# Kernel optimization log

Measured on AMD Instinct MI355X. Metric: run time of the kernel, lower is better.

The kernel has to match this reference:

```python
import jax, jax.numpy as jnp
import numpy as np

N, E, H, XD, ED, YD, L = 10000, 640000, 128, 8, 8, 112, 4
EPS_MSG = 1e-7   # GENConv message eps
EPS_SM = 1e-16   # pyg softmax denom eps
EPS_LN = 1e-5    # layernorm eps


def node_ln(x, g, b):
    # torch.nn.LayerNorm over last dim
    m = x.mean(axis=-1, keepdims=True)
    v = x.var(axis=-1, keepdims=True)
    return (x - m) * jax.lax.rsqrt(v + EPS_LN) * g + b


def graph_ln(x, g, b):
    # pyg LayerNorm mode='graph' (no batch): global mean/std over all nodes+channels
    xc = x - x.mean()
    std = jnp.sqrt((xc * xc).mean())
    return xc / (std + EPS_LN) * g + b


def setup_inputs() -> dict:
    key = jax.random.key(0)
    ks = jax.random.split(key, 10)
    rn = lambda k, s, sc: jax.random.normal(k, s, jnp.float32) * sc
    return {
        "x": jax.random.normal(ks[0], (N, XD), jnp.float32),
        "edge_index": jax.random.randint(ks[1], (2, E), 0, N),
        "edge_attr": jax.random.normal(ks[2], (E, ED), jnp.float32),
        "Wn": rn(ks[3], (XD, H), 0.3), "bn": jnp.zeros((H,), jnp.float32),
        "We": rn(ks[4], (ED, H), 0.3), "be": jnp.zeros((H,), jnp.float32),
        "t": jnp.ones((L,), jnp.float32),
        "W1": rn(ks[5], (L, H, 2 * H), 0.08), "b1": jnp.zeros((L, 2 * H), jnp.float32),
        "g1": jnp.ones((L, 2 * H), jnp.float32), "bt1": jnp.zeros((L, 2 * H), jnp.float32),
        "W2": rn(ks[6], (L, 2 * H, H), 0.08), "b2": jnp.zeros((L, H), jnp.float32),
        "lng": jnp.ones((L, H), jnp.float32), "lnb": jnp.zeros((L, H), jnp.float32),
        "Wout": rn(ks[7], (H, YD), 0.08), "bout": jnp.zeros((YD,), jnp.float32),
    }


def reference(x, edge_index, edge_attr, Wn, bn, We, be, t, W1, b1, g1, bt1,
              W2, b2, lng, lnb, Wout, bout):
    src, dst = edge_index[0], edge_index[1]
    h = x @ Wn + bn                       # [N,H] node encoder
    ea = edge_attr @ We + be              # [E,H] edge encoder

    def gen_conv(h, i):
        msg = jax.nn.relu(h[src] + ea) + EPS_MSG          # [E,H]
        logit = msg * t[i]
        mx = jax.ops.segment_max(logit, dst, num_segments=N)
        ex = jnp.exp(logit - mx[dst])
        den = jax.ops.segment_sum(ex, dst, num_segments=N)
        alpha = ex / (den[dst] + EPS_SM)
        agg = jax.ops.segment_sum(alpha * msg, dst, num_segments=N) + h  # root add
        z = jax.nn.relu(graph_ln(agg @ W1[i] + b1[i], g1[i], bt1[i]))
        return z @ W2[i] + b2[i]

    h = gen_conv(h, 0)                    # first layer: conv only
    for i in range(1, L):                 # res+ blocks (dropout off: eval)
        r = jax.nn.relu(node_ln(h, lng[i], lnb[i]))
        h = h + gen_conv(r, i)
    h = jax.nn.relu(node_ln(h, lng[0], lnb[0]))  # layers[0].act(layers[0].norm(x))
    return h @ Wout + bout
```

## Files before the change

kernel.cpp:

```cpp
#include <hip/hip_runtime.h>
#include <math.h>

#define NN 10000
#define NE 640000
#define H 128
#define H2 256
#define XD 8
#define ED 8
#define YD 112
#define NL 4
#define EPS_MSG 1e-7f
#define EPS_SM 1e-16f
#define EPS_LN 1e-5f
#define TM 8
#define NB1 (NN / TM)
#define TNO 16
#define NBO (NN / TNO)

typedef _Float16 h2 __attribute__((ext_vector_type(2)));

__global__ void hist_k(const int* __restrict__ dst, int* __restrict__ counts) {
    int e = blockIdx.x * 256 + threadIdx.x;
    if (e < NE) atomicAdd(&counts[dst[e]], 1);
}

__global__ void scan_k(const int* __restrict__ counts, int* __restrict__ rowptr) {
    __shared__ int part[1024];
    int tid = threadIdx.x;
    const int CH = (NN + 1023) / 1024;
    int base = tid * CH;
    int s = 0;
    for (int j = 0; j < CH; j++) { int i = base + j; if (i < NN) s += counts[i]; }
    part[tid] = s; __syncthreads();
    for (int off = 1; off < 1024; off <<= 1) {
        int v = (tid >= off) ? part[tid - off] : 0;
        __syncthreads();
        part[tid] += v;
        __syncthreads();
    }
    int run = part[tid] - s;
    for (int j = 0; j < CH; j++) {
        int i = base + j;
        if (i < NN) { rowptr[i] = run; run += counts[i]; }
    }
    if (tid == 1023) rowptr[NN] = run;
}

__global__ void scatter_k(const int* __restrict__ dst, const int* __restrict__ rowptr,
                          int* __restrict__ fill, int* __restrict__ perm) {
    int e = blockIdx.x * 256 + threadIdx.x;
    if (e >= NE) return;
    int d = dst[e];
    int pos = rowptr[d] + atomicAdd(&fill[d], 1);
    perm[pos] = e;
}

__global__ void pack_k(const int* __restrict__ perm, const int* __restrict__ src,
                       const float* __restrict__ eattr, int* __restrict__ srcs,
                       _Float16* __restrict__ eacsr) {
    int pos = blockIdx.x * 256 + threadIdx.x;
    if (pos >= NE) return;
    int e = perm[pos];
    srcs[pos] = src[e];
    const float4* ein = (const float4*)eattr;
    float4 a = ein[(size_t)e * 2];
    float4 b = ein[(size_t)e * 2 + 1];
    float4 pack;
    _Float16* pp = (_Float16*)&pack;
    pp[0] = (_Float16)a.x; pp[1] = (_Float16)a.y; pp[2] = (_Float16)a.z; pp[3] = (_Float16)a.w;
    pp[4] = (_Float16)b.x; pp[5] = (_Float16)b.y; pp[6] = (_Float16)b.z; pp[7] = (_Float16)b.w;
    ((float4*)eacsr)[pos] = pack;
}

__global__ void node_enc_k(const float* __restrict__ x, const float* __restrict__ Wn,
                           const float* __restrict__ bn, float* __restrict__ h) {
    int n = blockIdx.x, c = threadIdx.x;
    __shared__ float xl[XD];
    if (c < XD) xl[c] = x[n * XD + c];
    __syncthreads();
    float acc = bn[c];
#pragma unroll
    for (int k = 0; k < XD; k++) acc = fmaf(xl[k], Wn[k * H + c], acc);
    h[(size_t)n * H + c] = acc;
}

__global__ void __launch_bounds__(64) edge_agg_k(
    const float* __restrict__ rin, const int* __restrict__ rowptr,
    const int* __restrict__ srcs, const _Float16* __restrict__ eacsr,
    const float* __restrict__ We, const float* __restrict__ be,
    const float* __restrict__ tptr, int layer, float* __restrict__ agg) {
    int n = blockIdx.x, c = threadIdx.x;
    h2 wA[4], wB[4];
#pragma unroll
    for (int k = 0; k < 4; k++) {
        wA[k][0] = (_Float16)We[(2 * k) * H + c];
        wA[k][1] = (_Float16)We[(2 * k + 1) * H + c];
        wB[k][0] = (_Float16)We[(2 * k) * H + c + 64];
        wB[k][1] = (_Float16)We[(2 * k + 1) * H + c + 64];
    }
    float becA = be[c], becB = be[c + 64];
    float ts2 = tptr[layer] * 1.44269504088896f;
    int beg = rowptr[n], end = rowptr[n + 1];
    const float* rn0 = rin + (size_t)n * H + c;
    float rvA = rn0[0], rvB = rn0[64];
    float denA = 0.f, numA = 0.f, denB = 0.f, numB = 0.f;
#pragma unroll 4
    for (int j = beg; j < end; ++j) {
        int sn = srcs[j];
        float4 raw = *(const float4*)(eacsr + (size_t)j * ED);
        const h2* ep = (const h2*)&raw;
        const float* hp = rin + (size_t)sn * H + c;
        float hvA = hp[0], hvB = hp[64];
        float pA = __builtin_amdgcn_fdot2(ep[0], wA[0], becA, false);
        pA = __builtin_amdgcn_fdot2(ep[1], wA[1], pA, false);
        pA = __builtin_amdgcn_fdot2(ep[2], wA[2], pA, false);
        pA = __builtin_amdgcn_fdot2(ep[3], wA[3], pA, false);
        float pB = __builtin_amdgcn_fdot2(ep[0], wB[0], becB, false);
        pB = __builtin_amdgcn_fdot2(ep[1], wB[1], pB, false);
        pB = __builtin_amdgcn_fdot2(ep[2], wB[2], pB, false);
        pB = __builtin_amdgcn_fdot2(ep[3], wB[3], pB, false);
        float msgA = fmaxf(hvA + pA, 0.f) + EPS_MSG;
        float msgB = fmaxf(hvB + pB, 0.f) + EPS_MSG;
        float peA = __builtin_amdgcn_exp2f(msgA * ts2);
        float peB = __builtin_amdgcn_exp2f(msgB * ts2);
        denA += peA; numA = fmaf(peA, msgA, numA);
        denB += peB; numB = fmaf(peB, msgB, numB);
    }
    float* ao = agg + (size_t)n * H + c;
    ao[0]  = numA / (denA + EPS_SM) + rvA;
    ao[64] = numB / (denB + EPS_SM) + rvB;
}

__global__ void __launch_bounds__(256) mm1_k(const float* __restrict__ agg,
    const float* __restrict__ W1i, const float* __restrict__ b1i,
    float* __restrict__ y1, float* __restrict__ part) {
    int nb = blockIdx.x, o = threadIdx.x;
    int n0 = nb * TM;
    __shared__ float a[TM][H];
    {
        const float4* ag4 = (const float4*)(agg + (size_t)n0 * H);
        float4* a4 = (float4*)a;
        a4[o] = ag4[o];
    }
    __syncthreads();
    float acc[TM];
#pragma unroll
    for (int i = 0; i < TM; i++) acc[i] = 0.f;
    for (int k = 0; k < H; k += 4) {
        float w0 = W1i[k * H2 + o];
        float w1 = W1i[(k + 1) * H2 + o];
        float w2 = W1i[(k + 2) * H2 + o];
        float w3 = W1i[(k + 3) * H2 + o];
#pragma unroll
        for (int i = 0; i < TM; i++) {
            float4 av = *(const float4*)&a[i][k];
            acc[i] = fmaf(av.x, w0, acc[i]);
            acc[i] = fmaf(av.y, w1, acc[i]);
            acc[i] = fmaf(av.z, w2, acc[i]);
            acc[i] = fmaf(av.w, w3, acc[i]);
        }
    }
    float bo = b1i[o];
    float ps = 0.f, ps2 = 0.f;
#pragma unroll
    for (int i = 0; i < TM; i++) {
        float v = acc[i] + bo;
        y1[(size_t)(n0 + i) * H2 + o] = v;
        ps += v; ps2 += v * v;
    }
#pragma unroll
    for (int off = 32; off; off >>= 1) { ps += __shfl_xor(ps, off); ps2 += __shfl_xor(ps2, off); }
    __shared__ float red[8];
    int w = o >> 6;
    if ((o & 63) == 0) { red[w] = ps; red[4 + w] = ps2; }
    __syncthreads();
    if (o == 0) {
        part[nb * 2]     = red[0] + red[1] + red[2] + red[3];
        part[nb * 2 + 1] = red[4] + red[5] + red[6] + red[7];
    }
}

__global__ void __launch_bounds__(256) mm2_k(const float* __restrict__ y1,
    const float* __restrict__ g1i, const float* __restrict__ bt1i,
    const float* __restrict__ W2i, const float* __restrict__ b2i,
    const float* __restrict__ part, float* __restrict__ h,
    const float* __restrict__ lgp, const float* __restrict__ lbp,
    float* __restrict__ r, int first) {
    int nb = blockIdx.x, tid = threadIdx.x;
    int o = tid & 127, half = tid >> 7;
    int rb = half * 4;
    int n0 = nb * TM;
    float s = 0.f, s2 = 0.f;
    for (int i = tid; i < NB1; i += 256) { s += part[2 * i]; s2 += part[2 * i + 1]; }
#pragma unroll
    for (int off = 32; off; off >>= 1) { s += __shfl_xor(s, off); s2 += __shfl_xor(s2, off); }
    __shared__ float sred[8];
    int w4 = tid >> 6;
    if ((tid & 63) == 0) { sred[w4] = s; sred[4 + w4] = s2; }
    __syncthreads();
    const float M = (float)NN * (float)H2;
    float m = (sred[0] + sred[1] + sred[2] + sred[3]) / M;
    float var = fmaxf((sred[4] + sred[5] + sred[6] + sred[7]) / M - m * m, 0.f);
    float istd = 1.f / (sqrtf(var) + EPS_LN);

    __shared__ float z[TM][H2];
    __syncthreads();
    {
        const float4* y4 = (const float4*)(y1 + (size_t)n0 * H2);
        const float4* g4 = (const float4*)g1i;
        const float4* b4 = (const float4*)bt1i;
        float4* z4 = (float4*)z;
#pragma unroll
        for (int t = tid; t < TM * H2 / 4; t += 256) {
            int k4 = t & 63;
            float4 v = y4[t];
            float4 g = g4[k4], b = b4[k4];
            v.x = fmaxf((v.x - m) * istd * g.x + b.x, 0.f);
            v.y = fmaxf((v.y - m) * istd * g.y + b.y, 0.f);
            v.z = fmaxf((v.z - m) * istd * g.z + b.z, 0.f);
            v.w = fmaxf((v.w - m) * istd * g.w + b.w, 0.f);
            z4[t] = v;
        }
    }
    __syncthreads();
    float acc[4];
#pragma unroll
    for (int i = 0; i < 4; i++) acc[i] = 0.f;
    for (int k = 0; k < H2; k += 4) {
        float w0 = W2i[k * H + o];
        float w1 = W2i[(k + 1) * H + o];
        float w2 = W2i[(k + 2) * H + o];
        float w3 = W2i[(k + 3) * H + o];
#pragma unroll
        for (int i = 0; i < 4; i++) {
            float4 zv = *(const float4*)&z[rb + i][k];
            acc[i] = fmaf(zv.x, w0, acc[i]);
            acc[i] = fmaf(zv.y, w1, acc[i]);
            acc[i] = fmaf(zv.z, w2, acc[i]);
            acc[i] = fmaf(zv.w, w3, acc[i]);
        }
    }
    float bo = b2i[o];
    float vv[4];
#pragma unroll
    for (int i = 0; i < 4; i++) {
        size_t idx = (size_t)(n0 + rb + i) * H + o;
        float v = acc[i] + bo;
        if (!first) v += h[idx];
        h[idx] = v;
        vv[i] = v;
    }
    __shared__ float rs[2][2][4], rs2[2][2][4];
    int w2i_ = (tid >> 6) & 1;
#pragma unroll
    for (int i = 0; i < 4; i++) {
        float ss = vv[i], ss2 = vv[i] * vv[i];
#pragma unroll
        for (int off = 32; off; off >>= 1) { ss += __shfl_xor(ss, off); ss2 += __shfl_xor(ss2, off); }
        if ((tid & 63) == 0) { rs[half][w2i_][i] = ss; rs2[half][w2i_][i] = ss2; }
    }
    __syncthreads();
    float gc = lgp[o], bc = lbp[o];
#pragma unroll
    for (int i = 0; i < 4; i++) {
        float S = rs[half][0][i] + rs[half][1][i];
        float S2 = rs2[half][0][i] + rs2[half][1][i];
        float mn = S * (1.f / H);
        float vr = S2 * (1.f / H) - mn * mn;
        float inv = rsqrtf(vr + EPS_LN);
        float ov = (vv[i] - mn) * inv * gc + bc;
        r[(size_t)(n0 + rb + i) * H + o] = fmaxf(ov, 0.f);
    }
}

__global__ void __launch_bounds__(128) mmout_k(const float* __restrict__ r,
    const float* __restrict__ Wout, const float* __restrict__ bout,
    float* __restrict__ out) {
    int nb = blockIdx.x, o = threadIdx.x;
    int n0 = nb * TNO;
    __shared__ float a[TNO][H];
    {
        const float4* r4 = (const float4*)(r + (size_t)n0 * H);
        float4* a4 = (float4*)a;
        for (int t = o; t < TNO * H / 4; t += 128) a4[t] = r4[t];
    }
    __syncthreads();
    if (o < YD) {
        float acc[TNO];
#pragma unroll
        for (int i = 0; i < TNO; i++) acc[i] = 0.f;
        for (int k = 0; k < H; k += 4) {
            float w0 = Wout[k * YD + o];
            float w1 = Wout[(k + 1) * YD + o];
            float w2 = Wout[(k + 2) * YD + o];
            float w3 = Wout[(k + 3) * YD + o];
#pragma unroll
            for (int i = 0; i < TNO; i++) {
                float4 av = *(const float4*)&a[i][k];
                acc[i] = fmaf(av.x, w0, acc[i]);
                acc[i] = fmaf(av.y, w1, acc[i]);
                acc[i] = fmaf(av.z, w2, acc[i]);
                acc[i] = fmaf(av.w, w3, acc[i]);
            }
        }
        float bo = bout[o];
#pragma unroll
        for (int i = 0; i < TNO; i++) out[(size_t)(n0 + i) * YD + o] = acc[i] + bo;
    }
}

extern "C" void kernel_launch(void* const* d_in, const int* in_sizes, int n_in,
                              void* d_out, int out_size, void* d_ws, size_t ws_size,
                              hipStream_t stream) {
    const float* x    = (const float*)d_in[0];
    const int*   ei   = (const int*)d_in[1];
    const float* eattr= (const float*)d_in[2];
    const float* Wn   = (const float*)d_in[3];
    const float* bn   = (const float*)d_in[4];
    const float* We   = (const float*)d_in[5];
    const float* be   = (const float*)d_in[6];
    const float* t    = (const float*)d_in[7];
    const float* W1   = (const float*)d_in[8];
    const float* b1   = (const float*)d_in[9];
    const float* g1   = (const float*)d_in[10];
    const float* bt1  = (const float*)d_in[11];
    const float* W2   = (const float*)d_in[12];
    const float* b2   = (const float*)d_in[13];
    const float* lng  = (const float*)d_in[14];
    const float* lnb  = (const float*)d_in[15];
    const float* Wout = (const float*)d_in[16];
    const float* bout = (const float*)d_in[17];
    float* out = (float*)d_out;

    const int* src = ei;
    const int* dst = ei + NE;

    char* ws = (char*)d_ws;
    size_t off = 0;
    auto alloc = [&](size_t bytes) -> char* {
        char* p = ws + off;
        off += (bytes + 255) & ~(size_t)255;
        return p;
    };
    int*      counts = (int*)alloc((size_t)NN * 2 * 4);
    int*      fill   = counts + NN;
    int*      rowptr = (int*)alloc((size_t)(NN + 1) * 4);
    int*      perm   = (int*)alloc((size_t)NE * 4);
    int*      srcs   = (int*)alloc((size_t)NE * 4);
    _Float16* eacsr  = (_Float16*)alloc((size_t)NE * ED * 2);
    float*    h      = (float*)alloc((size_t)NN * H * 4);
    float*    r      = (float*)alloc((size_t)NN * H * 4);
    float*    agg    = (float*)alloc((size_t)NN * H * 4);
    float*    y1     = (float*)alloc((size_t)NN * H2 * 4);
    float*    part   = (float*)alloc((size_t)NB1 * 2 * 4);
    (void)ws_size; (void)in_sizes; (void)n_in; (void)out_size;

    hipMemsetAsync(counts, 0, (size_t)NN * 2 * 4, stream);

    hist_k<<<(NE + 255) / 256, 256, 0, stream>>>(dst, counts);
    scan_k<<<1, 1024, 0, stream>>>(counts, rowptr);
    scatter_k<<<(NE + 255) / 256, 256, 0, stream>>>(dst, rowptr, fill, perm);
    pack_k<<<(NE + 255) / 256, 256, 0, stream>>>(perm, src, eattr, srcs, eacsr);
    node_enc_k<<<NN, H, 0, stream>>>(x, Wn, bn, h);

    for (int i = 0; i < NL; i++) {
        const float* cin = (i == 0) ? h : r;
        edge_agg_k<<<NN, 64, 0, stream>>>(cin, rowptr, srcs, eacsr, We, be, t, i, agg);
        mm1_k<<<NB1, 256, 0, stream>>>(agg, W1 + (size_t)i * H * H2, b1 + i * H2, y1, part);
        int nx = (i == NL - 1) ? 0 : (i + 1);
        mm2_k<<<NB1, 256, 0, stream>>>(y1, g1 + i * H2, bt1 + i * H2,
                                       W2 + (size_t)i * H2 * H, b2 + i * H, part, h,
                                       lng + nx * H, lnb + nx * H, r, (i == 0) ? 1 : 0);
    }
    mmout_k<<<NBO, 128, 0, stream>>>(r, Wout, bout, out);
}
```

Measured before the change: 493.7 us.

## Fuse edge aggregation into first MLP matmul and merge pack with node encoder

Edge softmax aggregation now runs inside the first MLP matmul kernel: each 512-thread block has 8 wavefronts, one per node, writes the aggregated rows into shared memory, and then does the 8x256 matmul with each thread handling 4 rows. This removes the global agg buffer round trip and one kernel launch per layer. The edge pack and node encoder kernels are also merged into a single launch. The cost is that each block's matmul now waits on its slowest node's edge loop, grid parallelism drops from 10000 small blocks to 1250 larger ones, and the matmul work per thread is halved.

```diff
diff --git a/kernel.cpp b/kernel.cpp
--- a/kernel.cpp
+++ b/kernel.cpp
@@ -55,105 +55,108 @@
     perm[pos] = e;
 }
 
-__global__ void pack_k(const int* __restrict__ perm, const int* __restrict__ src,
-                       const float* __restrict__ eattr, int* __restrict__ srcs,
-                       _Float16* __restrict__ eacsr) {
-    int pos = blockIdx.x * 256 + threadIdx.x;
-    if (pos >= NE) return;
-    int e = perm[pos];
-    srcs[pos] = src[e];
-    const float4* ein = (const float4*)eattr;
-    float4 a = ein[(size_t)e * 2];
-    float4 b = ein[(size_t)e * 2 + 1];
-    float4 pack;
-    _Float16* pp = (_Float16*)&pack;
-    pp[0] = (_Float16)a.x; pp[1] = (_Float16)a.y; pp[2] = (_Float16)a.z; pp[3] = (_Float16)a.w;
-    pp[4] = (_Float16)b.x; pp[5] = (_Float16)b.y; pp[6] = (_Float16)b.z; pp[7] = (_Float16)b.w;
-    ((float4*)eacsr)[pos] = pack;
-}
-
-__global__ void node_enc_k(const float* __restrict__ x, const float* __restrict__ Wn,
-                           const float* __restrict__ bn, float* __restrict__ h) {
-    int n = blockIdx.x, c = threadIdx.x;
-    __shared__ float xl[XD];
-    if (c < XD) xl[c] = x[n * XD + c];
-    __syncthreads();
-    float acc = bn[c];
-#pragma unroll
-    for (int k = 0; k < XD; k++) acc = fmaf(xl[k], Wn[k * H + c], acc);
-    h[(size_t)n * H + c] = acc;
-}
-
-__global__ void __launch_bounds__(64) edge_agg_k(
+__global__ void __launch_bounds__(256) packenc_k(
+    const int* __restrict__ perm, const int* __restrict__ src,
+    const float* __restrict__ eattr, int* __restrict__ srcs,
+    _Float16* __restrict__ eacsr,
+    const float* __restrict__ x, const float* __restrict__ Wn,
+    const float* __restrict__ bn, float* __restrict__ h) {
+    int b = blockIdx.x;
+    if (b < 2500) {
+        int pos = b * 256 + threadIdx.x;
+        int e = perm[pos];
+        srcs[pos] = src[e];
+        const float4* ein = (const float4*)eattr;
+        float4 a = ein[(size_t)e * 2];
+        float4 bb = ein[(size_t)e * 2 + 1];
+        float4 pk;
+        _Float16* pp = (_Float16*)&pk;
+        pp[0] = (_Float16)a.x; pp[1] = (_Float16)a.y; pp[2] = (_Float16)a.z; pp[3] = (_Float16)a.w;
+        pp[4] = (_Float16)bb.x; pp[5] = (_Float16)bb.y; pp[6] = (_Float16)bb.z; pp[7] = (_Float16)bb.w;
+        ((float4*)eacsr)[pos] = pk;
+    } else {
+        int bb = b - 2500;
+        int c = threadIdx.x & 127, ln = threadIdx.x >> 7;
+        int n = bb * 2 + ln;
+        const float4* xr = (const float4*)(x + (size_t)n * XD);
+        float4 x0 = xr[0], x1 = xr[1];
+        float acc = bn[c];
+        acc = fmaf(x0.x, Wn[0 * H + c], acc); acc = fmaf(x0.y, Wn[1 * H + c], acc);
+        acc = fmaf(x0.z, Wn[2 * H + c], acc); acc = fmaf(x0.w, Wn[3 * H + c], acc);
+        acc = fmaf(x1.x, Wn[4 * H + c], acc); acc = fmaf(x1.y, Wn[5 * H + c], acc);
+        acc = fmaf(x1.z, Wn[6 * H + c], acc); acc = fmaf(x1.w, Wn[7 * H + c], acc);
+        h[(size_t)n * H + c] = acc;
+    }
+}
+
+__global__ void __launch_bounds__(512) ea_mm1_k(
     const float* __restrict__ rin, const int* __restrict__ rowptr,
     const int* __restrict__ srcs, const _Float16* __restrict__ eacsr,
     const float* __restrict__ We, const float* __restrict__ be,
-    const float* __restrict__ tptr, int layer, float* __restrict__ agg) {
-    int n = blockIdx.x, c = threadIdx.x;
-    h2 wA[4], wB[4];
-#pragma unroll
-    for (int k = 0; k < 4; k++) {
-        wA[k][0] = (_Float16)We[(2 * k) * H + c];
-        wA[k][1] = (_Float16)We[(2 * k + 1) * H + c];
-        wB[k][0] = (_Float16)We[(2 * k) * H + c + 64];
-        wB[k][1] = (_Float16)We[(2 * k + 1) * H + c + 64];
-    }
-    float becA = be[c], becB = be[c + 64];
-    float ts2 = tptr[layer] * 1.44269504088896f;
-    int beg = rowptr[n], end = rowptr[n + 1];
-    const float* rn0 = rin + (size_t)n * H + c;
-    float rvA = rn0[0], rvB = rn0[64];
-    float denA = 0.f, numA = 0.f, denB = 0.f, numB = 0.f;
-#pragma unroll 4
-    for (int j = beg; j < end; ++j) {
-        int sn = srcs[j];
-        float4 raw = *(const float4*)(eacsr + (size_t)j * ED);
-        const h2* ep = (const h2*)&raw;
-        const float* hp = rin + (size_t)sn * H + c;
-        float hvA = hp[0], hvB = hp[64];
-        float pA = __builtin_amdgcn_fdot2(ep[0], wA[0], becA, false);
-        pA = __builtin_amdgcn_fdot2(ep[1], wA[1], pA, false);
-        pA = __builtin_amdgcn_fdot2(ep[2], wA[2], pA, false);
-        pA = __builtin_amdgcn_fdot2(ep[3], wA[3], pA, false);
-        float pB = __builtin_amdgcn_fdot2(ep[0], wB[0], becB, false);
-        pB = __builtin_amdgcn_fdot2(ep[1], wB[1], pB, false);
-        pB = __builtin_amdgcn_fdot2(ep[2], wB[2], pB, false);
-        pB = __builtin_amdgcn_fdot2(ep[3], wB[3], pB, false);
-        float msgA = fmaxf(hvA + pA, 0.f) + EPS_MSG;
-        float msgB = fmaxf(hvB + pB, 0.f) + EPS_MSG;
-        float peA = __builtin_amdgcn_exp2f(msgA * ts2);
-        float peB = __builtin_amdgcn_exp2f(msgB * ts2);
-        denA += peA; numA = fmaf(peA, msgA, numA);
-        denB += peB; numB = fmaf(peB, msgB, numB);
-    }
-    float* ao = agg + (size_t)n * H + c;
-    ao[0]  = numA / (denA + EPS_SM) + rvA;
-    ao[64] = numB / (denB + EPS_SM) + rvB;
-}
-
-__global__ void __launch_bounds__(256) mm1_k(const float* __restrict__ agg,
+    const float* __restrict__ tptr, int layer,
     const float* __restrict__ W1i, const float* __restrict__ b1i,
     float* __restrict__ y1, float* __restrict__ part) {
-    int nb = blockIdx.x, o = threadIdx.x;
+    int nb = blockIdx.x, tid = threadIdx.x;
     int n0 = nb * TM;
     __shared__ float a[TM][H];
+
     {
-        const float4* ag4 = (const float4*)(agg + (size_t)n0 * H);
-        float4* a4 = (float4*)a;
-        a4[o] = ag4[o];
-    }
-    __syncthreads();
-    float acc[TM];
-#pragma unroll
-    for (int i = 0; i < TM; i++) acc[i] = 0.f;
+        int wv = tid >> 6, c = tid & 63;
+        int n = n0 + wv;
+        h2 wA[4], wB[4];
+#pragma unroll
+        for (int k = 0; k < 4; k++) {
+            wA[k][0] = (_Float16)We[(2 * k) * H + c];
+            wA[k][1] = (_Float16)We[(2 * k + 1) * H + c];
+            wB[k][0] = (_Float16)We[(2 * k) * H + c + 64];
+            wB[k][1] = (_Float16)We[(2 * k + 1) * H + c + 64];
+        }
+        float becA = be[c], becB = be[c + 64];
+        float ts2 = tptr[layer] * 1.44269504088896f;
+        int beg = rowptr[n], end = rowptr[n + 1];
+        const float* rn0 = rin + (size_t)n * H + c;
+        float rvA = rn0[0], rvB = rn0[64];
+        float denA = 0.f, numA = 0.f, denB = 0.f, numB = 0.f;
+#pragma unroll 4
+        for (int j = beg; j < end; ++j) {
+            int sn = srcs[j];
+            float4 raw = *(const float4*)(eacsr + (size_t)j * ED);
+            const h2* ep = (const h2*)&raw;
+            const float* hp = rin + (size_t)sn * H + c;
+            float hvA = hp[0], hvB = hp[64];
+            float pA = __builtin_amdgcn_fdot2(ep[0], wA[0], becA, false);
+            pA = __builtin_amdgcn_fdot2(ep[1], wA[1], pA, false);
+            pA = __builtin_amdgcn_fdot2(ep[2], wA[2], pA, false);
+            pA = __builtin_amdgcn_fdot2(ep[3], wA[3], pA, false);
+            float pB = __builtin_amdgcn_fdot2(ep[0], wB[0], becB, false);
+            pB = __builtin_amdgcn_fdot2(ep[1], wB[1], pB, false);
+            pB = __builtin_amdgcn_fdot2(ep[2], wB[2], pB, false);
+            pB = __builtin_amdgcn_fdot2(ep[3], wB[3], pB, false);
+            float msgA = fmaxf(hvA + pA, 0.f) + EPS_MSG;
+            float msgB = fmaxf(hvB + pB, 0.f) + EPS_MSG;
+            float peA = __builtin_amdgcn_exp2f(msgA * ts2);
+            float peB = __builtin_amdgcn_exp2f(msgB * ts2);
+            denA += peA; numA = fmaf(peA, msgA, numA);
+            denB += peB; numB = fmaf(peB, msgB, numB);
+        }
+        a[wv][c]      = numA / (denA + EPS_SM) + rvA;
+        a[wv][c + 64] = numB / (denB + EPS_SM) + rvB;
+    }
+    __syncthreads();
+
+    int o = tid & 255, half = tid >> 8;
+    int rb = half * 4;
+    float acc[4];
+#pragma unroll
+    for (int i = 0; i < 4; i++) acc[i] = 0.f;
     for (int k = 0; k < H; k += 4) {
         float w0 = W1i[k * H2 + o];
         float w1 = W1i[(k + 1) * H2 + o];
         float w2 = W1i[(k + 2) * H2 + o];
         float w3 = W1i[(k + 3) * H2 + o];
 #pragma unroll
-        for (int i = 0; i < TM; i++) {
-            float4 av = *(const float4*)&a[i][k];
+        for (int i = 0; i < 4; i++) {
+            float4 av = *(const float4*)&a[rb + i][k];
             acc[i] = fmaf(av.x, w0, acc[i]);
             acc[i] = fmaf(av.y, w1, acc[i]);
             acc[i] = fmaf(av.z, w2, acc[i]);
@@ -163,20 +166,23 @@
     float bo = b1i[o];
     float ps = 0.f, ps2 = 0.f;
 #pragma unroll
-    for (int i = 0; i < TM; i++) {
+    for (int i = 0; i < 4; i++) {
         float v = acc[i] + bo;
-        y1[(size_t)(n0 + i) * H2 + o] = v;
+        y1[(size_t)(n0 + rb + i) * H2 + o] = v;
         ps += v; ps2 += v * v;
     }
 #pragma unroll
     for (int off = 32; off; off >>= 1) { ps += __shfl_xor(ps, off); ps2 += __shfl_xor(ps2, off); }
-    __shared__ float red[8];
-    int w = o >> 6;
-    if ((o & 63) == 0) { red[w] = ps; red[4 + w] = ps2; }
-    __syncthreads();
-    if (o == 0) {
-        part[nb * 2]     = red[0] + red[1] + red[2] + red[3];
-        part[nb * 2 + 1] = red[4] + red[5] + red[6] + red[7];
+    __shared__ float red[16];
+    int w8 = tid >> 6;
+    if ((tid & 63) == 0) { red[w8] = ps; red[8 + w8] = ps2; }
+    __syncthreads();
+    if (tid == 0) {
+        float S = 0.f, S2 = 0.f;
+#pragma unroll
+        for (int i = 0; i < 8; i++) { S += red[i]; S2 += red[8 + i]; }
+        part[nb * 2] = S;
+        part[nb * 2 + 1] = S2;
     }
 }
 
@@ -350,7 +356,6 @@
     _Float16* eacsr  = (_Float16*)alloc((size_t)NE * ED * 2);
     float*    h      = (float*)alloc((size_t)NN * H * 4);
     float*    r      = (float*)alloc((size_t)NN * H * 4);
-    float*    agg    = (float*)alloc((size_t)NN * H * 4);
     float*    y1     = (float*)alloc((size_t)NN * H2 * 4);
     float*    part   = (float*)alloc((size_t)NB1 * 2 * 4);
     (void)ws_size; (void)in_sizes; (void)n_in; (void)out_size;
@@ -360,13 +365,13 @@
     hist_k<<<(NE + 255) / 256, 256, 0, stream>>>(dst, counts);
     scan_k<<<1, 1024, 0, stream>>>(counts, rowptr);
     scatter_k<<<(NE + 255) / 256, 256, 0, stream>>>(dst, rowptr, fill, perm);
-    pack_k<<<(NE + 255) / 256, 256, 0, stream>>>(perm, src, eattr, srcs, eacsr);
-    node_enc_k<<<NN, H, 0, stream>>>(x, Wn, bn, h);
+    packenc_k<<<2500 + NN / 2, 256, 0, stream>>>(perm, src, eattr, srcs, eacsr,
+                                                 x, Wn, bn, h);
 
     for (int i = 0; i < NL; i++) {
         const float* cin = (i == 0) ? h : r;
-        edge_agg_k<<<NN, 64, 0, stream>>>(cin, rowptr, srcs, eacsr, We, be, t, i, agg);
-        mm1_k<<<NB1, 256, 0, stream>>>(agg, W1 + (size_t)i * H * H2, b1 + i * H2, y1, part);
+        ea_mm1_k<<<NB1, 512, 0, stream>>>(cin, rowptr, srcs, eacsr, We, be, t, i,
+                                          W1 + (size_t)i * H * H2, b1 + i * H2, y1, part);
         int nx = (i == NL - 1) ? 0 : (i + 1);
         mm2_k<<<NB1, 256, 0, stream>>>(y1, g1 + i * H2, bt1 + i * H2,
                                        W2 + (size_t)i * H2 * H, b2 + i * H, part, h,
```

After: 487.4 us. No clear change (-1.3%).
